# Kernel tuning notes

Measured on AMD Instinct MI355X. Metric: run time of the kernel, lower is better.

Reference implementation:

```python
import jax, jax.numpy as jnp
import numpy as np

N = 50000
E = 800000
D = 128
NEG_SLOPE = 0.2


def _gat_layer(x, W, al, ar, b, src, dst):
    """Single-head DGL-style GATConv with ReLU activation."""
    z = x @ W                                    # [N, D] projected features
    el = z @ al                                  # [N] left attention logits
    er = z @ ar                                  # [N] right attention logits
    e = jax.nn.leaky_relu(el[src] + er[dst], NEG_SLOPE)   # [E]
    # softmax over incoming edges per destination node (numerically stable)
    m = jax.ops.segment_max(e, dst, num_segments=N)       # [N]
    ex = jnp.exp(e - m[dst])                               # [E]
    s = jax.ops.segment_sum(ex, dst, num_segments=N)       # [N]
    alpha = ex / s[dst]                                    # [E]
    out = jax.ops.segment_sum(alpha[:, None] * z[src], dst, num_segments=N)  # [N, D]
    return jax.nn.relu(out + b)


def setup_inputs() -> dict:
    key = jax.random.key(0)
    ks = jax.random.split(key, 16)
    s = 0.05
    inp = {
        "f": jax.random.normal(ks[0], (N, D), dtype=jnp.float32),
        "src": jax.random.randint(ks[1], (E,), 0, N, dtype=jnp.int32),
        "dst": jax.random.randint(ks[2], (E,), 0, N, dtype=jnp.int32),
    }
    for i, kb in zip((1, 2, 3), (3, 7, 11)):
        inp[f"W{i}"] = jax.random.normal(ks[kb], (D, D), dtype=jnp.float32) * s
        inp[f"al{i}"] = jax.random.normal(ks[kb + 1], (D,), dtype=jnp.float32) * s
        inp[f"ar{i}"] = jax.random.normal(ks[kb + 2], (D,), dtype=jnp.float32) * s
        inp[f"b{i}"] = jnp.zeros((D,), dtype=jnp.float32)
    return inp


def reference(f, src, dst, W1, al1, ar1, b1, W2, al2, ar2, b2, W3, al3, ar3, b3):
    h = _gat_layer(f, W1, al1, ar1, b1, src, dst)
    h = _gat_layer(h, W2, al2, ar2, b2, src, dst)
    h = _gat_layer(h, W3, al3, ar3, b3, src, dst)
    return h  # [N, D] (single head already squeezed)
```

## Files before the change

### kernel.cpp

```cpp
#include <hip/hip_runtime.h>
#include <hip/hip_fp16.h>
#include <math.h>

#define NN 50000
#define NE 800000
#define DD 128
#define NEG_SLOPE 0.2f
#define CAP 64
#define GBLK ((NN + 63) / 64)
#define WSBLK (3 * 16384 / 256)
#define HBLK ((NE + 255) / 256)
#define SBLK ((NE + 511) / 512)
#define AQBLK (NN / 16)

typedef short frag8 __attribute__((ext_vector_type(8)));
typedef float f32x4 __attribute__((ext_vector_type(4)));

__device__ __forceinline__ unsigned bf16_rne(float x) {
  unsigned u = __float_as_uint(x);
  return (u + 0x7FFFu + ((u >> 16) & 1u)) >> 16;
}

__device__ __forceinline__ void wsplit_body(
    int bid, const float* __restrict__ W0, const float* __restrict__ W1,
    const float* __restrict__ W2, short* __restrict__ Wh, short* __restrict__ Wl) {
  int gidx = bid * 256 + threadIdx.x;
  int L = gidx >> 14;
  int idx = gidx & 16383;
  const float* W = (L == 0) ? W0 : (L == 1) ? W1 : W2;
  int j = idx & 7;
  int lane = (idx >> 3) & 63;
  int tile = idx >> 9;
  int nt = tile & 7, kt = tile >> 3;
  int k = kt * 32 + (lane >> 4) * 8 + j;
  int n = nt * 16 + (lane & 15);
  float x = W[k * DD + n];
  unsigned hu = bf16_rne(x);
  float hf = __uint_as_float(hu << 16);
  unsigned lu = bf16_rne(x - hf);
  Wh[gidx] = (short)hu;
  Wl[gidx] = (short)lu;
}

__device__ __forceinline__ void hist_body(int bid, const int* __restrict__ dst,
                                          int* __restrict__ deg,
                                          unsigned short* __restrict__ edge_slot) {
  int i = bid * 256 + threadIdx.x;
  if (i < NE) edge_slot[i] = (unsigned short)atomicAdd(&deg[dst[i]], 1);
}

__global__ __launch_bounds__(256) void fused_pre(
    const float* __restrict__ W0, const float* __restrict__ W1, const float* __restrict__ W2,
    short* __restrict__ Wh, short* __restrict__ Wl,
    const int* __restrict__ dst, int* __restrict__ deg,
    unsigned short* __restrict__ edge_slot) {
  if (blockIdx.x < WSBLK) wsplit_body(blockIdx.x, W0, W1, W2, Wh, Wl);
  else hist_body(blockIdx.x - WSBLK, dst, deg, edge_slot);
}

__device__ __forceinline__ void gemm_body(
    int bid, short (*sB)[8192], float (*elp)[64], float (*erp)[64],
    const float* __restrict__ x, const short* __restrict__ Wh, const short* __restrict__ Wl,
    const float* __restrict__ al, const float* __restrict__ ar,
    __half* __restrict__ z, float* __restrict__ el, float* __restrict__ er) {
  const int t = threadIdx.x;
  const int w = t >> 6, lane = t & 63;
  const int m = lane & 15, quad = lane >> 4;
  const int half = w >> 2, mw = w & 3;
  const int ntb = half * 4;
  const int R0 = bid * 64 + mw * 16;

  auto stage = [&](int kt, int buf) {
    const uint4* gh = (const uint4*)(Wh + kt * 4096);
    const uint4* gl = (const uint4*)(Wl + kt * 4096);
    uint4* s = (uint4*)sB[buf];
    s[t] = gh[t];
    s[t + 512] = gl[t];
  };

  f32x4 acc[4];
#pragma unroll
  for (int n = 0; n < 4; n++) acc[n] = (f32x4)(0.f);

  int rA = R0 + m; if (rA > NN - 1) rA = NN - 1;

  stage(0, 0);
  __syncthreads();

#pragma unroll
  for (int kt = 0; kt < 4; kt++) {
    const int buf = kt & 1;
    if (kt < 3) stage(kt + 1, buf ^ 1);

    const float* xp = x + (size_t)rA * DD + kt * 32 + quad * 8;
    float xv[8];
    *(float4*)(xv) = *(const float4*)xp;
    *(float4*)(xv + 4) = *(const float4*)(xp + 4);
    frag8 ah, alo;
#pragma unroll
    for (int j = 0; j < 8; j++) {
      unsigned hu = bf16_rne(xv[j]);
      float hf = __uint_as_float(hu << 16);
      ah[j] = (short)hu;
      alo[j] = (short)bf16_rne(xv[j] - hf);
    }
#pragma unroll
    for (int n = 0; n < 4; n++) {
      frag8 bh = *(const frag8*)&sB[buf][(ntb + n) * 512 + lane * 8];
      frag8 bl = *(const frag8*)&sB[buf][4096 + (ntb + n) * 512 + lane * 8];
      acc[n] = __builtin_amdgcn_mfma_f32_16x16x32_bf16(alo, bh, acc[n], 0, 0, 0);
      acc[n] = __builtin_amdgcn_mfma_f32_16x16x32_bf16(ah, bl, acc[n], 0, 0, 0);
      acc[n] = __builtin_amdgcn_mfma_f32_16x16x32_bf16(ah, bh, acc[n], 0, 0, 0);
    }
    __syncthreads();
  }

  float alv[4], arv[4];
#pragma unroll
  for (int n = 0; n < 4; n++) {
    alv[n] = al[(ntb + n) * 16 + m];
    arv[n] = ar[(ntb + n) * 16 + m];
  }
#pragma unroll
  for (int r = 0; r < 4; r++) {
    float pl = 0.f, pr = 0.f;
#pragma unroll
    for (int n = 0; n < 4; n++) { pl += acc[n][r] * alv[n]; pr += acc[n][r] * arv[n]; }
#pragma unroll
    for (int off = 8; off; off >>= 1) {
      pl += __shfl_xor(pl, off, 64);
      pr += __shfl_xor(pr, off, 64);
    }
    int lrow = mw * 16 + quad * 4 + r;
    if (m == 0) { elp[half][lrow] = pl; erp[half][lrow] = pr; }
    int row = R0 + quad * 4 + r;
    if (row < NN) {
#pragma unroll
      for (int n = 0; n < 4; n++) {
        unsigned short hu = __half_as_ushort(__float2half(acc[n][r]));
        unsigned short hn = (unsigned short)__shfl_xor((int)hu, 1, 64);
        if ((m & 1) == 0) {
          int col0 = (ntb + n) * 16 + m;
          __half2 pair = __halves2half2(__ushort_as_half(hu), __ushort_as_half(hn));
          *(__half2*)(z + (size_t)(col0 >> 5) * NN * 32 + (size_t)row * 32 + (col0 & 31)) = pair;
        }
      }
    }
  }
  __syncthreads();
  if (t < 64) {
    int row = bid * 64 + t;
    if (row < NN) {
      el[row] = elp[0][t] + elp[1][t];
      er[row] = erp[0][t] + erp[1][t];
    }
  }
}

__device__ __forceinline__ void scatter_body(
    int bid, const int* __restrict__ src, const int* __restrict__ dst,
    const unsigned short* __restrict__ edge_slot, unsigned short* __restrict__ csr_src) {
  int i = bid * 512 + threadIdx.x;
  if (i >= NE) return;
  int slot = edge_slot[i]; if (slot > CAP - 1) slot = CAP - 1;
  csr_src[dst[i] * CAP + slot] = (unsigned short)src[i];
}

__global__ __launch_bounds__(512) void gemm_mfma(
    const float* __restrict__ x, const short* __restrict__ Wh, const short* __restrict__ Wl,
    const float* __restrict__ al, const float* __restrict__ ar,
    __half* __restrict__ z, float* __restrict__ el, float* __restrict__ er) {
  __shared__ __align__(16) short sB[2][8192];
  __shared__ float elp[2][64], erp[2][64];
  gemm_body(blockIdx.x, sB, elp, erp, x, Wh, Wl, al, ar, z, el, er);
}

__global__ __launch_bounds__(512) void fused_scatter_gemm(
    const float* __restrict__ x, const short* __restrict__ Wh, const short* __restrict__ Wl,
    const float* __restrict__ al, const float* __restrict__ ar,
    __half* __restrict__ z, float* __restrict__ el, float* __restrict__ er,
    const int* __restrict__ src, const int* __restrict__ dst,
    const unsigned short* __restrict__ edge_slot, unsigned short* __restrict__ csr_src) {
  __shared__ __align__(16) short sB[2][8192];
  __shared__ float elp[2][64], erp[2][64];
  if (blockIdx.x < GBLK) gemm_body(blockIdx.x, sB, elp, erp, x, Wh, Wl, al, ar, z, el, er);
  else scatter_body(blockIdx.x - GBLK, src, dst, edge_slot, csr_src);
}

__global__ __launch_bounds__(256) void gat_agg(
    const int* __restrict__ deg, const unsigned short* __restrict__ csr_src,
    const float* __restrict__ el, const float* __restrict__ er,
    const __half* __restrict__ z, const float* __restrict__ b,
    float* __restrict__ out) {
  const int bid = blockIdx.x;
  const int q = bid / AQBLK;
  const int nb = bid - q * AQBLK;
  const int t = threadIdx.x;
  const int g = t >> 4;
  const int l0 = t & 15;
  const int node = nb * 16 + g;
  int dn = deg[node]; if (dn > CAP) dn = CAP;
  const int beg = node * CAP;
  const float erd = er[node];
  const __half2* zq = (const __half2*)(z + (size_t)q * NN * 32) + l0;

  int sn[4]; float wv[4]; float ssum = 0.f;
#pragma unroll
  for (int i = 0; i < 4; i++) {
    int e = i * 16 + l0;
    sn[i] = 0; wv[i] = 0.f;
    if (e < dn) {
      sn[i] = csr_src[beg + e];
      float ev = el[sn[i]] + erd;
      ev = (ev > 0.f) ? ev : NEG_SLOPE * ev;
      wv[i] = __expf(ev);
      ssum += wv[i];
    }
  }
#pragma unroll
  for (int off = 8; off; off >>= 1) ssum += __shfl_xor(ssum, off, 64);
  float inv_s = (dn > 0) ? 1.f / ssum : 0.f;

  float2 acc = make_float2(0.f, 0.f);
#pragma unroll
  for (int i = 0; i < 4; i++) {
    int lim = dn - i * 16;
    if (lim <= 0) break;
    int cnt = min(16, lim);
    for (int jj = 0; jj < cnt; jj += 8) {
      float ww[8]; int ss[8];
#pragma unroll
      for (int u = 0; u < 8; u++) {
        ww[u] = __shfl(wv[i], g * 16 + jj + u, 64);
        ss[u] = __shfl(sn[i], g * 16 + jj + u, 64);
      }
      float2 zv[8];
#pragma unroll
      for (int u = 0; u < 8; u++) zv[u] = __half22float2(zq[(size_t)ss[u] * 16]);
#pragma unroll
      for (int u = 0; u < 8; u++) { acc.x += ww[u] * zv[u].x; acc.y += ww[u] * zv[u].y; }
    }
  }

  float2 bv = *(const float2*)(b + q * 32 + l0 * 2);
  float ox = fmaxf(acc.x * inv_s + bv.x, 0.f);
  float oy = fmaxf(acc.y * inv_s + bv.y, 0.f);
  *(float2*)(out + (size_t)node * DD + q * 32 + l0 * 2) = make_float2(ox, oy);
}

extern "C" void kernel_launch(void* const* d_in, const int* in_sizes, int n_in,
                              void* d_out, int out_size, void* d_ws, size_t ws_size,
                              hipStream_t stream) {
  const float* f   = (const float*)d_in[0];
  const int*   src = (const int*)d_in[1];
  const int*   dst = (const int*)d_in[2];
  const float* W[3]  = {(const float*)d_in[3], (const float*)d_in[7],  (const float*)d_in[11]};
  const float* al[3] = {(const float*)d_in[4], (const float*)d_in[8],  (const float*)d_in[12]};
  const float* ar[3] = {(const float*)d_in[5], (const float*)d_in[9],  (const float*)d_in[13]};
  const float* bb[3] = {(const float*)d_in[6], (const float*)d_in[10], (const float*)d_in[14]};

  short* Wh3 = (short*)d_ws;
  short* Wl3 = Wh3 + 3 * 16384;
  __half* zbuf = (__half*)(Wl3 + 3 * 16384);
  float* hbuf = (float*)(zbuf + (size_t)NN * DD);
  float* el = hbuf + (size_t)NN * DD;
  float* er = el + NN;
  int* deg = (int*)(er + NN);
  unsigned short* edge_slot = (unsigned short*)(deg + NN);
  unsigned short* csr_src   = edge_slot + NE;

  hipMemsetAsync(deg, 0, NN * sizeof(int), stream);
  fused_pre<<<WSBLK + HBLK, 256, 0, stream>>>(W[0], W[1], W[2], Wh3, Wl3, dst, deg, edge_slot);
  fused_scatter_gemm<<<GBLK + SBLK, 512, 0, stream>>>(f, Wh3, Wl3, al[0], ar[0],
                                                      zbuf, el, er,
                                                      src, dst, edge_slot, csr_src);
  gat_agg<<<4 * AQBLK, 256, 0, stream>>>(deg, csr_src, el, er, zbuf, bb[0], hbuf);

  gemm_mfma<<<GBLK, 512, 0, stream>>>(hbuf, Wh3 + 16384, Wl3 + 16384,
                                      al[1], ar[1], zbuf, el, er);
  gat_agg<<<4 * AQBLK, 256, 0, stream>>>(deg, csr_src, el, er, zbuf, bb[1], hbuf);

  gemm_mfma<<<GBLK, 512, 0, stream>>>(hbuf, Wh3 + 2 * 16384, Wl3 + 2 * 16384,
                                      al[2], ar[2], zbuf, el, er);
  gat_agg<<<4 * AQBLK, 256, 0, stream>>>(deg, csr_src, el, er, zbuf, bb[2],
                                         (float*)d_out);
}
```

Before: 319.7 us.

## Precompute per-edge attention weights once instead of per feature quarter

Adds an edge_w kernel that computes the exp attention weights and the per-node softmax normaliser once per layer, storing packed (weight, src) pairs in a padded per-node buffer. gat_agg then reads these pairs directly, with no shuffles and no per-quarter recomputation, where before the weights were recomputed by each of the four feature-quarter blocks. The cost is an extra kernel launch per layer and extra global traffic to write and read the 8-byte packed buffer (NN*CAP entries).

```diff
diff --git a/kernel.cpp b/kernel.cpp
--- a/kernel.cpp
+++ b/kernel.cpp
@@ -12,6 +12,7 @@
 #define HBLK ((NE + 255) / 256)
 #define SBLK ((NE + 511) / 512)
 #define AQBLK (NN / 16)
+#define EWBLK (NN / 16)
 
 typedef short frag8 __attribute__((ext_vector_type(8)));
 typedef float f32x4 __attribute__((ext_vector_type(4)));
@@ -187,11 +188,41 @@
   else scatter_body(blockIdx.x - GBLK, src, dst, edge_slot, csr_src);
 }
 
-__global__ __launch_bounds__(256) void gat_agg(
+__global__ __launch_bounds__(256) void edge_w(
     const int* __restrict__ deg, const unsigned short* __restrict__ csr_src,
     const float* __restrict__ el, const float* __restrict__ er,
-    const __half* __restrict__ z, const float* __restrict__ b,
-    float* __restrict__ out) {
+    float2* __restrict__ pkbuf, float* __restrict__ inv_s) {
+  const int t = threadIdx.x;
+  const int g = t >> 4, l0 = t & 15;
+  const int node = blockIdx.x * 16 + g;
+  int dn = deg[node]; if (dn > CAP) dn = CAP;
+  const int dn8 = (dn + 7) & ~7;
+  const int beg = node * CAP;
+  const float erd = er[node];
+  float ssum = 0.f;
+#pragma unroll
+  for (int i = 0; i < 4; i++) {
+    int e = i * 16 + l0;
+    if (e < dn) {
+      int sn = csr_src[beg + e];
+      float ev = el[sn] + erd;
+      ev = (ev > 0.f) ? ev : NEG_SLOPE * ev;
+      float w = __expf(ev);
+      ssum += w;
+      pkbuf[beg + e] = make_float2(w, __uint_as_float((unsigned)sn));
+    } else if (e < dn8) {
+      pkbuf[beg + e] = make_float2(0.f, __uint_as_float(0u));
+    }
+  }
+#pragma unroll
+  for (int off = 8; off; off >>= 1) ssum += __shfl_xor(ssum, off, 64);
+  if (l0 == 0) inv_s[node] = (dn > 0) ? 1.f / ssum : 0.f;
+}
+
+__global__ __launch_bounds__(256) void gat_agg(
+    const int* __restrict__ deg, const float2* __restrict__ pkbuf,
+    const float* __restrict__ inv_s, const __half* __restrict__ z,
+    const float* __restrict__ b, float* __restrict__ out) {
   const int bid = blockIdx.x;
   const int q = bid / AQBLK;
   const int nb = bid - q * AQBLK;
@@ -200,51 +231,27 @@
   const int l0 = t & 15;
   const int node = nb * 16 + g;
   int dn = deg[node]; if (dn > CAP) dn = CAP;
+  const int dn8 = (dn + 7) & ~7;
   const int beg = node * CAP;
-  const float erd = er[node];
   const __half2* zq = (const __half2*)(z + (size_t)q * NN * 32) + l0;
 
-  int sn[4]; float wv[4]; float ssum = 0.f;
-#pragma unroll
-  for (int i = 0; i < 4; i++) {
-    int e = i * 16 + l0;
-    sn[i] = 0; wv[i] = 0.f;
-    if (e < dn) {
-      sn[i] = csr_src[beg + e];
-      float ev = el[sn[i]] + erd;
-      ev = (ev > 0.f) ? ev : NEG_SLOPE * ev;
-      wv[i] = __expf(ev);
-      ssum += wv[i];
-    }
-  }
-#pragma unroll
-  for (int off = 8; off; off >>= 1) ssum += __shfl_xor(ssum, off, 64);
-  float inv_s = (dn > 0) ? 1.f / ssum : 0.f;
-
   float2 acc = make_float2(0.f, 0.f);
-#pragma unroll
-  for (int i = 0; i < 4; i++) {
-    int lim = dn - i * 16;
-    if (lim <= 0) break;
-    int cnt = min(16, lim);
-    for (int jj = 0; jj < cnt; jj += 8) {
-      float ww[8]; int ss[8];
-#pragma unroll
-      for (int u = 0; u < 8; u++) {
-        ww[u] = __shfl(wv[i], g * 16 + jj + u, 64);
-        ss[u] = __shfl(sn[i], g * 16 + jj + u, 64);
-      }
-      float2 zv[8];
-#pragma unroll
-      for (int u = 0; u < 8; u++) zv[u] = __half22float2(zq[(size_t)ss[u] * 16]);
-#pragma unroll
-      for (int u = 0; u < 8; u++) { acc.x += ww[u] * zv[u].x; acc.y += ww[u] * zv[u].y; }
-    }
-  }
-
+  for (int jj = 0; jj < dn8; jj += 8) {
+    float2 pk[8];
+#pragma unroll
+    for (int u = 0; u < 8; u++) pk[u] = pkbuf[beg + jj + u];
+    float2 zv[8];
+#pragma unroll
+    for (int u = 0; u < 8; u++)
+      zv[u] = __half22float2(zq[(size_t)__float_as_uint(pk[u].y) * 16]);
+#pragma unroll
+    for (int u = 0; u < 8; u++) { acc.x += pk[u].x * zv[u].x; acc.y += pk[u].x * zv[u].y; }
+  }
+
+  float is = inv_s[node];
   float2 bv = *(const float2*)(b + q * 32 + l0 * 2);
-  float ox = fmaxf(acc.x * inv_s + bv.x, 0.f);
-  float oy = fmaxf(acc.y * inv_s + bv.y, 0.f);
+  float ox = fmaxf(acc.x * is + bv.x, 0.f);
+  float oy = fmaxf(acc.y * is + bv.y, 0.f);
   *(float2*)(out + (size_t)node * DD + q * 32 + l0 * 2) = make_float2(ox, oy);
 }
 
@@ -265,8 +272,10 @@
   float* hbuf = (float*)(zbuf + (size_t)NN * DD);
   float* el = hbuf + (size_t)NN * DD;
   float* er = el + NN;
-  int* deg = (int*)(er + NN);
-  unsigned short* edge_slot = (unsigned short*)(deg + NN);
+  float* inv_s = er + NN;
+  int* deg = (int*)(inv_s + NN);
+  float2* pkbuf = (float2*)(deg + NN);
+  unsigned short* edge_slot = (unsigned short*)(pkbuf + (size_t)NN * CAP);
   unsigned short* csr_src   = edge_slot + NE;
 
   hipMemsetAsync(deg, 0, NN * sizeof(int), stream);
@@ -274,14 +283,17 @@
   fused_scatter_gemm<<<GBLK + SBLK, 512, 0, stream>>>(f, Wh3, Wl3, al[0], ar[0],
                                                       zbuf, el, er,
                                                       src, dst, edge_slot, csr_src);
-  gat_agg<<<4 * AQBLK, 256, 0, stream>>>(deg, csr_src, el, er, zbuf, bb[0], hbuf);
+  edge_w<<<EWBLK, 256, 0, stream>>>(deg, csr_src, el, er, pkbuf, inv_s);
+  gat_agg<<<4 * AQBLK, 256, 0, stream>>>(deg, pkbuf, inv_s, zbuf, bb[0], hbuf);
 
   gemm_mfma<<<GBLK, 512, 0, stream>>>(hbuf, Wh3 + 16384, Wl3 + 16384,
                                       al[1], ar[1], zbuf, el, er);
-  gat_agg<<<4 * AQBLK, 256, 0, stream>>>(deg, csr_src, el, er, zbuf, bb[1], hbuf);
+  edge_w<<<EWBLK, 256, 0, stream>>>(deg, csr_src, el, er, pkbuf, inv_s);
+  gat_agg<<<4 * AQBLK, 256, 0, stream>>>(deg, pkbuf, inv_s, zbuf, bb[1], hbuf);
 
   gemm_mfma<<<GBLK, 512, 0, stream>>>(hbuf, Wh3 + 2 * 16384, Wl3 + 2 * 16384,
                                       al[2], ar[2], zbuf, el, er);
-  gat_agg<<<4 * AQBLK, 256, 0, stream>>>(deg, csr_src, el, er, zbuf, bb[2],
+  edge_w<<<EWBLK, 256, 0, stream>>>(deg, csr_src, el, er, pkbuf, inv_s);
+  gat_agg<<<4 * AQBLK, 256, 0, stream>>>(deg, pkbuf, inv_s, zbuf, bb[2],
                                          (float*)d_out);
 }
```

Result: slower. 329.5 us (+3.1%).
